# Performance work log

Measured on AMD Instinct MI355X. Metric: run time of the kernel, lower is better.

Reference implementation:

```python
import jax, jax.numpy as jnp
import numpy as np
from jax import lax

VOCAB = 50000; EMB = 128; HID = 256; NL = 9; B = 128; T = 512; H = HID // 2; PAD = 0


def setup_inputs() -> dict:
    key = jax.random.key(0)
    ks = jax.random.split(key, 16)
    p = lambda k, s: jax.random.normal(k, s, jnp.float32) * 0.05
    return {
        "chars": jax.random.randint(ks[0], (B, T), 1, VOCAB),  # in [1, VOCAB) so mask fully on
        "labels": jax.random.randint(ks[1], (B, T), 0, NL),
        "emb": p(ks[2], (VOCAB, EMB)),
        "W_ih_f": p(ks[3], (4 * H, EMB)), "W_hh_f": p(ks[4], (4 * H, H)),
        "b_ih_f": p(ks[5], (4 * H,)), "b_hh_f": p(ks[6], (4 * H,)),
        "W_ih_b": p(ks[7], (4 * H, EMB)), "W_hh_b": p(ks[8], (4 * H, H)),
        "b_ih_b": p(ks[9], (4 * H,)), "b_hh_b": p(ks[10], (4 * H,)),
        "W_out": p(ks[11], (NL, HID)), "b_out": p(ks[12], (NL,)),
        "start_trans": p(ks[13], (NL,)), "end_trans": p(ks[14], (NL,)),
        "trans": p(ks[15], (NL, NL)),
    }


def _lstm(x, Wih, Whh, bih, bhh, reverse):
    # x: (B, T, D); PyTorch gate order i, f, g, o
    bsz = x.shape[0]
    h0 = jnp.zeros((bsz, H), x.dtype)
    c0 = jnp.zeros((bsz, H), x.dtype)
    b = bih + bhh

    def step(carry, xt):
        h, c = carry
        g = xt @ Wih.T + h @ Whh.T + b  # (B, 4H)
        i, f, gg, o = jnp.split(g, 4, axis=-1)
        c = jax.nn.sigmoid(f) * c + jax.nn.sigmoid(i) * jnp.tanh(gg)
        h = jax.nn.sigmoid(o) * jnp.tanh(c)
        return (h, c), h

    _, hs = lax.scan(step, (h0, c0), jnp.swapaxes(x, 0, 1), reverse=reverse)
    return jnp.swapaxes(hs, 0, 1)  # (B, T, H)


def _crf_nll(emissions, labels, mask, start, end, trans):
    # torchcrf linear-chain CRF log-likelihood, reduction='sum'
    maskf = mask.astype(emissions.dtype)
    emit = jnp.take_along_axis(emissions, labels[..., None], 2)[..., 0]  # (B, T)
    score = start[labels[:, 0]] + (emit * maskf).sum(1)
    score = score + (trans[labels[:, :-1], labels[:, 1:]] * maskf[:, 1:]).sum(1)
    last_idx = mask.sum(1).astype(jnp.int32) - 1
    last_tags = jnp.take_along_axis(labels, last_idx[:, None], 1)[:, 0]
    score = score + end[last_tags]

    # forward algorithm (log partition) as a scan over time
    alpha0 = start[None, :] + emissions[:, 0]  # (B, L)

    def step(alpha, inp):
        e_t, m_t = inp  # (B, L), (B,)
        nxt = jax.nn.logsumexp(alpha[:, :, None] + trans[None, :, :], axis=1) + e_t
        return jnp.where(m_t[:, None], nxt, alpha), None

    alpha, _ = lax.scan(step, alpha0,
                        (jnp.swapaxes(emissions, 0, 1)[1:], jnp.swapaxes(mask, 0, 1)[1:]))
    logZ = jax.nn.logsumexp(alpha + end[None, :], axis=-1)
    return -(score - logZ).sum()


def reference(chars, labels, emb, W_ih_f, W_hh_f, b_ih_f, b_hh_f,
              W_ih_b, W_hh_b, b_ih_b, b_hh_b, W_out, b_out,
              start_trans, end_trans, trans):
    x = emb[chars]  # (B, T, EMB)
    hf = _lstm(x, W_ih_f, W_hh_f, b_ih_f, b_hh_f, False)
    hb = _lstm(x, W_ih_b, W_hh_b, b_ih_b, b_hh_b, True)
    h = jnp.concatenate([hf, hb], axis=-1)  # (B, T, HID)
    emissions = h @ W_out.T + b_out  # dropout is identity in eval mode
    mask = chars != PAD
    return _crf_nll(emissions, labels, mask, start_trans, end_trans, trans)
```

## Files before the change

kernel.cpp:

```cpp
#include <hip/hip_runtime.h>

#define B_   128
#define T_   512
#define EMB_ 128
#define H_   128
#define NL_  9
#define MT_  65536

typedef __attribute__((ext_vector_type(8))) short short8v;
typedef __attribute__((ext_vector_type(4))) float float4v;

__device__ inline unsigned short f2bf(float f){
  unsigned u = __float_as_uint(f);
  u += 0x7FFFu + ((u >> 16) & 1u);
  return (unsigned short)(u >> 16);
}
__device__ inline float bf2f(unsigned short s){
  return __uint_as_float(((unsigned)s) << 16);
}
__device__ inline float sigm(float x){ return 1.f / (1.f + __expf(-x)); }
__device__ inline float tanh_(float x){ return 2.f / (1.f + __expf(-2.f * x)) - 1.f; }

#define LOG2E 1.44269504f
__device__ inline float vexp2(float x){ float r; asm("v_exp_f32 %0, %1" : "=v"(r) : "v"(x)); return r; }
__device__ inline float vrcp (float x){ float r; asm("v_rcp_f32 %0, %1" : "=v"(r) : "v"(x)); return r; }

__device__ inline float lstm_cell(float pi, float pf, float pg, float po, float& c){
  float ei = vexp2(-LOG2E * pi);
  float ef = vexp2(-LOG2E * pf);
  float eg = vexp2( 2.f * LOG2E * pg);
  float eo = vexp2(-LOG2E * po);
  float R1 = vrcp((1.f + ei) * (1.f + eg));
  float ig = (eg - 1.f) * R1;
  float F  = vrcp(1.f + ef);
  c = fmaf(F, c, ig);
  float ec = vexp2(2.f * LOG2E * c);
  float R2 = vrcp((1.f + eo) * (1.f + ec));
  return (ec - 1.f) * R2;
}

__device__ inline void gload16(const void* g, void* l){
  __builtin_amdgcn_global_load_lds(
      (const __attribute__((address_space(1))) void*)g,
      (__attribute__((address_space(3)))       void*)l, 16, 0, 0);
}

__global__ void k0_prep(const float* __restrict__ Wihf, const float* __restrict__ Whhf,
                        const float* __restrict__ bihf, const float* __restrict__ bhhf,
                        const float* __restrict__ Wihb, const float* __restrict__ Whhb,
                        const float* __restrict__ bihb, const float* __restrict__ bhhb,
                        unsigned short* __restrict__ Wih2, unsigned short* __restrict__ Whh2,
                        float* __restrict__ biasc){
  int blk = blockIdx.x;
  int dir = blk >> 9;
  int nd  = blk & 511;
  int k   = threadIdx.x;
  int j = nd >> 2, g = nd & 3;
  int orig = g * 128 + j;
  const float* Wih = dir ? Wihb : Wihf;
  const float* Whh = dir ? Whhb : Whhf;
  Wih2[((long)(dir * 512 + nd)) * 128 + k] = f2bf(Wih[orig * EMB_ + k]);
  Whh2[((long)(dir * 512 + nd)) * 128 + k] = f2bf(Whh[orig * H_ + k]);
  if (k == 0){
    const float* bi = dir ? bihb : bihf;
    const float* bh = dir ? bhhb : bhhf;
    biasc[dir * 512 + nd] = bi[orig] + bh[orig];
  }
}

__global__ void k1_embed(const int* __restrict__ chars, const float* __restrict__ emb,
                         unsigned short* __restrict__ x){
  int i = blockIdx.x * blockDim.x + threadIdx.x;
  int m = i >> 5, q = i & 31;
  int c = chars[m];
  const float4* e4 = (const float4*)(emb + (long)c * EMB_);
  float4 v = e4[q];
  ushort4 o;
  o.x = f2bf(v.x); o.y = f2bf(v.y); o.z = f2bf(v.z); o.w = f2bf(v.w);
  *(ushort4*)(x + (long)m * EMB_ + q * 4) = o;
}

#define CST 130
__global__ __launch_bounds__(256) void k2_gemm(const unsigned short* __restrict__ x,
                                               const unsigned short* __restrict__ Wih2,
                                               const float* __restrict__ biasc,
                                               unsigned short* __restrict__ G){
  __shared__ unsigned short gsm[64 * CST];
  int w = threadIdx.x >> 6, lane = threadIdx.x & 63;
  int r = lane & 15, kb = (lane >> 4) * 8;
  long arow = (long)(blockIdx.x * 64 + w * 16 + r);
  short8v a[4];
  #pragma unroll
  for (int kf = 0; kf < 4; kf++)
    a[kf] = *(const short8v*)(x + arow * EMB_ + kf * 32 + kb);
  int ncol0 = blockIdx.y * 128;
  float4v acc[8];
  #pragma unroll
  for (int nf = 0; nf < 8; nf++){
    float4v z = {0.f, 0.f, 0.f, 0.f};
    acc[nf] = z;
    int wrow = ncol0 + nf * 16 + r;
    #pragma unroll
    for (int kf = 0; kf < 4; kf++){
      short8v bfrag = *(const short8v*)(Wih2 + (long)wrow * 128 + kf * 32 + kb);
      acc[nf] = __builtin_amdgcn_mfma_f32_16x16x32_bf16(a[kf], bfrag, acc[nf], 0, 0, 0);
    }
  }
  int rloc0 = w * 16 + (lane >> 4) * 4;
  #pragma unroll
  for (int nf = 0; nf < 8; nf++){
    int col = ncol0 + nf * 16 + r;
    float bia = biasc[col];
    #pragma unroll
    for (int reg = 0; reg < 4; reg++)
      gsm[(rloc0 + reg) * CST + nf * 16 + r] = f2bf(acc[nf][reg] + bia);
  }
  __syncthreads();
  #pragma unroll
  for (int it = 0; it < 4; it++){
    int u = it * 256 + threadIdx.x;
    int row = u >> 4, cu = u & 15;
    short8v v = *(const short8v*)&gsm[row * CST + cu * 8];
    *(short8v*)(G + (long)(blockIdx.x * 64 + row) * 1024 + ncol0 + cu * 8) = v;
  }
}

#define HBST 136
#define GSTR 520
__global__ __launch_bounds__(1024, 1) void k3_scan3(
    const unsigned short* __restrict__ G,
    const unsigned short* __restrict__ Whh2,
    unsigned short* __restrict__ hs)
{
  const int blk = blockIdx.x;
  const int dir = blk >> 3;
  const int b0  = (blk & 7) * 16;
  const int tid = threadIdx.x;
  const int w   = tid >> 6;
  const int l   = tid & 63;
  const int r   = l & 15;
  const int q   = l >> 4;

  __shared__ unsigned short hR[4][16 * HBST];
  __shared__ unsigned short Gl[2][16 * GSTR];

  short8v Wf[2][4];
  #pragma unroll
  for (int t = 0; t < 2; t++){
    const unsigned short* wp = Whh2 + ((long)(dir * 512 + 32 * w + 16 * t + r)) * 128 + q * 8;
    #pragma unroll
    for (int kf = 0; kf < 4; kf++)
      Wf[t][kf] = *(const short8v*)(wp + kf * 32);
  }

  for (int i = tid; i < 16 * HBST; i += 1024) hR[3][i] = 0;

  float cc0 = 0.f, cc1 = 0.f;
  const int j0 = 8 * w + q;
  const int j1 = j0 + 4;

  const unsigned short* Gp0 = G + ((long)(b0 + w) * T_ + (dir ? T_ - 1 : 0)) * 1024
                                + dir * 512 + l * 8;
  const long gstep = (dir ? -1L : 1L) * 1024;
  const unsigned short* Gp = Gp0 + gstep;

  gload16(Gp0, &Gl[0][w * GSTR]);
  __syncthreads();

  for (int s = 0; s < T_; s++){
    const int p = s & 1;
    if (s + 1 < T_){
      gload16(Gp, &Gl[p ^ 1][w * GSTR]);
      Gp += gstep;
    }

    const unsigned short* hrow = &hR[(s + 3) & 3][r * HBST + q * 8];
    short8v hf0 = *(const short8v*)(hrow);
    short8v hf1 = *(const short8v*)(hrow + 32);
    short8v hf2 = *(const short8v*)(hrow + 64);
    short8v hf3 = *(const short8v*)(hrow + 96);

    ushort4 gp0 = *(const ushort4*)&Gl[p][r * GSTR + 32 * w + 4 * q];
    ushort4 gp1 = *(const ushort4*)&Gl[p][r * GSTR + 32 * w + 16 + 4 * q];
    float4v acc0 = {bf2f(gp0.x), bf2f(gp0.y), bf2f(gp0.z), bf2f(gp0.w)};
    float4v acc1 = {bf2f(gp1.x), bf2f(gp1.y), bf2f(gp1.z), bf2f(gp1.w)};

    acc0 = __builtin_amdgcn_mfma_f32_16x16x32_bf16(Wf[0][0], hf0, acc0, 0, 0, 0);
    acc0 = __builtin_amdgcn_mfma_f32_16x16x32_bf16(Wf[0][1], hf1, acc0, 0, 0, 0);
    acc0 = __builtin_amdgcn_mfma_f32_16x16x32_bf16(Wf[0][2], hf2, acc0, 0, 0, 0);
    acc0 = __builtin_amdgcn_mfma_f32_16x16x32_bf16(Wf[0][3], hf3, acc0, 0, 0, 0);
    acc1 = __builtin_amdgcn_mfma_f32_16x16x32_bf16(Wf[1][0], hf0, acc1, 0, 0, 0);
    acc1 = __builtin_amdgcn_mfma_f32_16x16x32_bf16(Wf[1][1], hf1, acc1, 0, 0, 0);
    acc1 = __builtin_amdgcn_mfma_f32_16x16x32_bf16(Wf[1][2], hf2, acc1, 0, 0, 0);
    acc1 = __builtin_amdgcn_mfma_f32_16x16x32_bf16(Wf[1][3], hf3, acc1, 0, 0, 0);

    float hv0 = lstm_cell(acc0[0], acc0[1], acc0[2], acc0[3], cc0);
    float hv1 = lstm_cell(acc1[0], acc1[1], acc1[2], acc1[3], cc1);

    unsigned pk;
    asm("v_cvt_pk_bf16_f32 %0, %1, %2" : "=v"(pk) : "v"(hv0), "v"(hv1));
    unsigned short* wrow = &hR[s & 3][r * HBST];
    wrow[j0] = (unsigned short)pk;
    wrow[j1] = (unsigned short)(pk >> 16);
    __syncthreads();

    if ((s & 3) == 3){
      int ii = tid >> 8, mm = (tid >> 4) & 15, j8 = tid & 15;
      int sg = s - 3 + ii;
      int tg = dir ? (T_ - 1 - sg) : sg;
      short8v v = *(const short8v*)&hR[ii][mm * HBST + j8 * 8];
      *(short8v*)(hs + ((long)dir * MT_ + (long)(b0 + mm) * T_ + tg) * H_ + j8 * 8) = v;
      __syncthreads();
    }
  }
}

#define HSTR 264
__global__ __launch_bounds__(512) void k4_emis(const unsigned short* __restrict__ hs,
                                               const float* __restrict__ Wout,
                                               const float* __restrict__ bout,
                                               float* __restrict__ em){
  __shared__ float hcat[64 * HSTR];
  __shared__ float wo[NL_ * 256];
  int tid = threadIdx.x;
  int m0 = blockIdx.x * 64;
  const unsigned short* hf = hs;
  const unsigned short* hb = hs + (long)MT_ * H_;
  #pragma unroll
  for (int it = 0; it < 8; it++){
    int flat = it * 2048 + tid * 4;
    int r = flat >> 8, u = flat & 255;
    const unsigned short* src = (u < 128) ? (hf + (long)(m0 + r) * H_ + u)
                                          : (hb + (long)(m0 + r) * H_ + (u - 128));
    ushort4 v = *(const ushort4*)src;
    hcat[r * HSTR + u]     = bf2f(v.x);
    hcat[r * HSTR + u + 1] = bf2f(v.y);
    hcat[r * HSTR + u + 2] = bf2f(v.z);
    hcat[r * HSTR + u + 3] = bf2f(v.w);
  }
  for (int f = tid; f < NL_ * 256; f += 512) wo[f] = Wout[f];
  __syncthreads();
  #pragma unroll
  for (int half = 0; half < 2; half++){
    int idx = half * 512 + tid;
    if (idx < 64 * NL_){
      int r = idx / NL_, lbl = idx % NL_;
      float acc = bout[lbl];
      #pragma unroll 8
      for (int u = 0; u < 256; u++)
        acc = fmaf(hcat[r * HSTR + u], wo[lbl * 256 + u], acc);
      em[(long)(m0 + r) * NL_ + lbl] = acc;
    }
  }
}

__global__ void k5_crf(const float* __restrict__ em, const int* __restrict__ chars,
                       const int* __restrict__ labels, const float* __restrict__ startv,
                       const float* __restrict__ endv, const float* __restrict__ trans,
                       float* __restrict__ partial){
  int b = blockIdx.x, lane = threadIdx.x;
  const int* lab = labels + b * T_;
  const int* ch  = chars + b * T_;
  const float* e = em + (long)b * T_ * NL_;
  float sc = 0.f; int cnt = 0;
  for (int t = lane; t < T_; t += 64){
    int m = (ch[t] != 0);
    cnt += m;
    if (m){
      sc += e[t * NL_ + lab[t]];
      if (t > 0) sc += trans[lab[t - 1] * NL_ + lab[t]];
    }
  }
  #pragma unroll
  for (int off = 32; off; off >>= 1){
    sc  += __shfl_down(sc, off);
    cnt += __shfl_down(cnt, off);
  }
  sc  = __shfl(sc, 0);
  cnt = __shfl(cnt, 0);
  if (cnt < 1) cnt = 1;
  int jl = (lane < NL_) ? lane : 0;
  float tcol[NL_];
  #pragma unroll
  for (int i = 0; i < NL_; i++) tcol[i] = trans[i * NL_ + jl];
  float alpha = (lane < NL_) ? (startv[jl] + e[jl]) : -1e30f;
  float evn = (lane < NL_) ? e[NL_ + jl] : 0.f;
  int   mn  = (ch[1] != 0);
  for (int t = 1; t < T_; t++){
    float ev = evn; int m = mn;
    int t2 = (t + 1 < T_) ? t + 1 : t;
    evn = (lane < NL_) ? e[t2 * NL_ + jl] : 0.f;
    mn  = (ch[t2] != 0);
    float vv[NL_]; float mx = -1e30f;
    #pragma unroll
    for (int i = 0; i < NL_; i++){
      vv[i] = __shfl(alpha, i) + tcol[i];
      mx = fmaxf(mx, vv[i]);
    }
    float ssum = 0.f;
    #pragma unroll
    for (int i = 0; i < NL_; i++) ssum += __expf(vv[i] - mx);
    float nxt = mx + __logf(ssum) + ev;
    if (m && lane < NL_) alpha = nxt;
  }
  float av = (lane < NL_) ? (alpha + endv[jl]) : -1e30f;
  float mx = av;
  #pragma unroll
  for (int off = 8; off; off >>= 1) mx = fmaxf(mx, __shfl_down(mx, off));
  mx = __shfl(mx, 0);
  float ex = (lane < NL_) ? __expf(av - mx) : 0.f;
  #pragma unroll
  for (int off = 8; off; off >>= 1) ex += __shfl_down(ex, off);
  if (lane == 0){
    float logZ = mx + __logf(ex);
    float score = sc + startv[lab[0]] + endv[lab[cnt - 1]];
    partial[b] = logZ - score;
  }
}

__global__ void k6_reduce(const float* __restrict__ partial, float* __restrict__ out){
  int lane = threadIdx.x;
  float v = partial[lane];
  #pragma unroll
  for (int off = 32; off; off >>= 1) v += __shfl_down(v, off);
  __shared__ float tmp[2];
  if ((lane & 63) == 0) tmp[lane >> 6] = v;
  __syncthreads();
  if (lane == 0) out[0] = tmp[0] + tmp[1];
}

extern "C" void kernel_launch(void* const* d_in, const int* in_sizes, int n_in,
                              void* d_out, int out_size, void* d_ws, size_t ws_size,
                              hipStream_t stream){
  const int*   chars  = (const int*)d_in[0];
  const int*   labels = (const int*)d_in[1];
  const float* emb    = (const float*)d_in[2];
  const float* Wihf   = (const float*)d_in[3];
  const float* Whhf   = (const float*)d_in[4];
  const float* bihf   = (const float*)d_in[5];
  const float* bhhf   = (const float*)d_in[6];
  const float* Wihb   = (const float*)d_in[7];
  const float* Whhb   = (const float*)d_in[8];
  const float* bihb   = (const float*)d_in[9];
  const float* bhhb   = (const float*)d_in[10];
  const float* Wout   = (const float*)d_in[11];
  const float* bout   = (const float*)d_in[12];
  const float* startv = (const float*)d_in[13];
  const float* endv   = (const float*)d_in[14];
  const float* trans  = (const float*)d_in[15];

  char* ws = (char*)d_ws;
  unsigned short* x     = (unsigned short*)(ws);
  float*          em    = (float*)         (ws);
  float*          part  = (float*)         (ws + 2359296);
  unsigned short* Wih2  = (unsigned short*)(ws + 16777216);
  unsigned short* Whh2  = (unsigned short*)(ws + 17301504);
  float*          biasc = (float*)         (ws + 17825792);
  unsigned short* G     = (unsigned short*)(ws + 17829888);
  unsigned short* hs    = (unsigned short*)(ws + 152047616);

  hipLaunchKernelGGL(k0_prep,  dim3(1024), dim3(128), 0, stream,
                     Wihf, Whhf, bihf, bhhf, Wihb, Whhb, bihb, bhhb, Wih2, Whh2, biasc);
  hipLaunchKernelGGL(k1_embed, dim3(8192), dim3(256), 0, stream, chars, emb, x);
  hipLaunchKernelGGL(k2_gemm,  dim3(1024, 8), dim3(256), 0, stream, x, Wih2, biasc, G);
  hipLaunchKernelGGL(k3_scan3, dim3(16),   dim3(1024), 0, stream, G, Whh2, hs);
  hipLaunchKernelGGL(k4_emis,  dim3(1024), dim3(512), 0, stream, hs, Wout, bout, em);
  hipLaunchKernelGGL(k5_crf,   dim3(128),  dim3(64),  0, stream,
                     em, chars, labels, startv, endv, trans, part);
  hipLaunchKernelGGL(k6_reduce, dim3(1),   dim3(128), 0, stream, part, (float*)d_out);
}
```

Measured before the change: 957.8 us.

## Prefetch gate inputs to registers and use lightweight LDS-only barriers in LSTM scan

The recurrent scan kernel no longer stages precomputed gate inputs through LDS with async global-to-LDS loads. Each lane now loads its own gate values straight into registers, two steps ahead, in double-buffered register sets. The history buffer grows to 8 slots so the hs flush to global memory happens once per 4 steps without its own extra barrier. Per-step __syncthreads is replaced by a barrier that waits only on LDS counters, which keeps the global loads in flight across steps. The risks are more register pressure and more exposed global load latency if the prefetch distance is too short.

```diff
diff --git a/kernel.cpp b/kernel.cpp
--- a/kernel.cpp
+++ b/kernel.cpp
@@ -18,8 +18,6 @@
 __device__ inline float bf2f(unsigned short s){
   return __uint_as_float(((unsigned)s) << 16);
 }
-__device__ inline float sigm(float x){ return 1.f / (1.f + __expf(-x)); }
-__device__ inline float tanh_(float x){ return 2.f / (1.f + __expf(-2.f * x)) - 1.f; }
 
 #define LOG2E 1.44269504f
 __device__ inline float vexp2(float x){ float r; asm("v_exp_f32 %0, %1" : "=v"(r) : "v"(x)); return r; }
@@ -39,10 +37,12 @@
   return (ec - 1.f) * R2;
 }
 
-__device__ inline void gload16(const void* g, void* l){
-  __builtin_amdgcn_global_load_lds(
-      (const __attribute__((address_space(1))) void*)g,
-      (__attribute__((address_space(3)))       void*)l, 16, 0, 0);
+__device__ inline void bar(){
+  __builtin_amdgcn_sched_barrier(0);
+  asm volatile("s_waitcnt lgkmcnt(0)" ::: "memory");
+  __builtin_amdgcn_sched_barrier(0);
+  __builtin_amdgcn_s_barrier();
+  __builtin_amdgcn_sched_barrier(0);
 }
 
 __global__ void k0_prep(const float* __restrict__ Wihf, const float* __restrict__ Whhf,
@@ -126,8 +126,7 @@
 }
 
 #define HBST 136
-#define GSTR 520
-__global__ __launch_bounds__(1024, 1) void k3_scan3(
+__global__ __launch_bounds__(1024, 1) void k3_scan4(
     const unsigned short* __restrict__ G,
     const unsigned short* __restrict__ Whh2,
     unsigned short* __restrict__ hs)
@@ -141,8 +140,7 @@
   const int r   = l & 15;
   const int q   = l >> 4;
 
-  __shared__ unsigned short hR[4][16 * HBST];
-  __shared__ unsigned short Gl[2][16 * GSTR];
+  __shared__ unsigned short hR[8][16 * HBST];
 
   short8v Wf[2][4];
   #pragma unroll
@@ -152,67 +150,83 @@
     for (int kf = 0; kf < 4; kf++)
       Wf[t][kf] = *(const short8v*)(wp + kf * 32);
   }
-
-  for (int i = tid; i < 16 * HBST; i += 1024) hR[3][i] = 0;
+  #pragma unroll
+  for (int t = 0; t < 2; t++)
+    #pragma unroll
+    for (int kf = 0; kf < 4; kf++)
+      asm volatile("" : "+v"(Wf[t][kf]));
+
+  for (int i = tid; i < 16 * HBST; i += 1024) hR[7][i] = 0;
 
   float cc0 = 0.f, cc1 = 0.f;
   const int j0 = 8 * w + q;
   const int j1 = j0 + 4;
-
-  const unsigned short* Gp0 = G + ((long)(b0 + w) * T_ + (dir ? T_ - 1 : 0)) * 1024
-                                + dir * 512 + l * 8;
-  const long gstep = (dir ? -1L : 1L) * 1024;
-  const unsigned short* Gp = Gp0 + gstep;
-
-  gload16(Gp0, &Gl[0][w * GSTR]);
-  __syncthreads();
-
-  for (int s = 0; s < T_; s++){
-    const int p = s & 1;
-    if (s + 1 < T_){
-      gload16(Gp, &Gl[p ^ 1][w * GSTR]);
-      Gp += gstep;
-    }
-
-    const unsigned short* hrow = &hR[(s + 3) & 3][r * HBST + q * 8];
-    short8v hf0 = *(const short8v*)(hrow);
-    short8v hf1 = *(const short8v*)(hrow + 32);
-    short8v hf2 = *(const short8v*)(hrow + 64);
-    short8v hf3 = *(const short8v*)(hrow + 96);
-
-    ushort4 gp0 = *(const ushort4*)&Gl[p][r * GSTR + 32 * w + 4 * q];
-    ushort4 gp1 = *(const ushort4*)&Gl[p][r * GSTR + 32 * w + 16 + 4 * q];
-    float4v acc0 = {bf2f(gp0.x), bf2f(gp0.y), bf2f(gp0.z), bf2f(gp0.w)};
-    float4v acc1 = {bf2f(gp1.x), bf2f(gp1.y), bf2f(gp1.z), bf2f(gp1.w)};
-
-    acc0 = __builtin_amdgcn_mfma_f32_16x16x32_bf16(Wf[0][0], hf0, acc0, 0, 0, 0);
-    acc0 = __builtin_amdgcn_mfma_f32_16x16x32_bf16(Wf[0][1], hf1, acc0, 0, 0, 0);
-    acc0 = __builtin_amdgcn_mfma_f32_16x16x32_bf16(Wf[0][2], hf2, acc0, 0, 0, 0);
-    acc0 = __builtin_amdgcn_mfma_f32_16x16x32_bf16(Wf[0][3], hf3, acc0, 0, 0, 0);
-    acc1 = __builtin_amdgcn_mfma_f32_16x16x32_bf16(Wf[1][0], hf0, acc1, 0, 0, 0);
-    acc1 = __builtin_amdgcn_mfma_f32_16x16x32_bf16(Wf[1][1], hf1, acc1, 0, 0, 0);
-    acc1 = __builtin_amdgcn_mfma_f32_16x16x32_bf16(Wf[1][2], hf2, acc1, 0, 0, 0);
-    acc1 = __builtin_amdgcn_mfma_f32_16x16x32_bf16(Wf[1][3], hf3, acc1, 0, 0, 0);
-
-    float hv0 = lstm_cell(acc0[0], acc0[1], acc0[2], acc0[3], cc0);
-    float hv1 = lstm_cell(acc1[0], acc1[1], acc1[2], acc1[3], cc1);
-
-    unsigned pk;
-    asm("v_cvt_pk_bf16_f32 %0, %1, %2" : "=v"(pk) : "v"(hv0), "v"(hv1));
-    unsigned short* wrow = &hR[s & 3][r * HBST];
-    wrow[j0] = (unsigned short)pk;
-    wrow[j1] = (unsigned short)(pk >> 16);
-    __syncthreads();
-
-    if ((s & 3) == 3){
-      int ii = tid >> 8, mm = (tid >> 4) & 15, j8 = tid & 15;
-      int sg = s - 3 + ii;
-      int tg = dir ? (T_ - 1 - sg) : sg;
-      short8v v = *(const short8v*)&hR[ii][mm * HBST + j8 * 8];
-      *(short8v*)(hs + ((long)dir * MT_ + (long)(b0 + mm) * T_ + tg) * H_ + j8 * 8) = v;
-      __syncthreads();
-    }
-  }
+  const int fii = tid >> 8, fmm = (tid >> 4) & 15, fj8 = tid & 15;
+
+  const long gstep = dir ? -1024L : 1024L;
+  const unsigned short* gbase = G + ((long)(b0 + r) * T_ + (dir ? T_ - 1 : 0)) * 1024
+                                  + dir * 512 + 32 * w + 4 * q;
+
+#define ISSUEX(D0A, D0B, D1A, D1B, S) do{                          \
+    const unsigned short* p_ = gbase + (long)(S) * gstep;          \
+    D0A = *(const ushort4*)(p_);                                   \
+    D0B = *(const ushort4*)(p_ + 16);                              \
+    D1A = *(const ushort4*)(p_ + gstep);                           \
+    D1B = *(const ushort4*)(p_ + gstep + 16);                      \
+  }while(0)
+
+#define STEPX(S, GA, GB) do{                                       \
+    const int slot_r = ((S) + 7) & 7, slot_w = (S) & 7;            \
+    const unsigned short* hrow = &hR[slot_r][r * HBST + q * 8];    \
+    short8v hf0 = *(const short8v*)(hrow);                         \
+    short8v hf1 = *(const short8v*)(hrow + 32);                    \
+    short8v hf2 = *(const short8v*)(hrow + 64);                    \
+    short8v hf3 = *(const short8v*)(hrow + 96);                    \
+    float4v acc0 = {bf2f((GA).x), bf2f((GA).y), bf2f((GA).z), bf2f((GA).w)}; \
+    float4v acc1 = {bf2f((GB).x), bf2f((GB).y), bf2f((GB).z), bf2f((GB).w)}; \
+    acc0 = __builtin_amdgcn_mfma_f32_16x16x32_bf16(Wf[0][0], hf0, acc0, 0, 0, 0); \
+    acc0 = __builtin_amdgcn_mfma_f32_16x16x32_bf16(Wf[0][1], hf1, acc0, 0, 0, 0); \
+    acc0 = __builtin_amdgcn_mfma_f32_16x16x32_bf16(Wf[0][2], hf2, acc0, 0, 0, 0); \
+    acc0 = __builtin_amdgcn_mfma_f32_16x16x32_bf16(Wf[0][3], hf3, acc0, 0, 0, 0); \
+    acc1 = __builtin_amdgcn_mfma_f32_16x16x32_bf16(Wf[1][0], hf0, acc1, 0, 0, 0); \
+    acc1 = __builtin_amdgcn_mfma_f32_16x16x32_bf16(Wf[1][1], hf1, acc1, 0, 0, 0); \
+    acc1 = __builtin_amdgcn_mfma_f32_16x16x32_bf16(Wf[1][2], hf2, acc1, 0, 0, 0); \
+    acc1 = __builtin_amdgcn_mfma_f32_16x16x32_bf16(Wf[1][3], hf3, acc1, 0, 0, 0); \
+    float hv0 = lstm_cell(acc0[0], acc0[1], acc0[2], acc0[3], cc0);\
+    float hv1 = lstm_cell(acc1[0], acc1[1], acc1[2], acc1[3], cc1);\
+    unsigned pk_;                                                  \
+    asm("v_cvt_pk_bf16_f32 %0, %1, %2" : "=v"(pk_) : "v"(hv0), "v"(hv1)); \
+    unsigned short* wr = &hR[slot_w][r * HBST];                    \
+    wr[j0] = (unsigned short)(pk_ & 0xffffu);                      \
+    wr[j1] = (unsigned short)(pk_ >> 16);                          \
+    bar();                                                         \
+  }while(0)
+
+#define FLUSHX(S4) do{                                             \
+    int sg_ = (S4) - 4 + fii;                                      \
+    int tg_ = dir ? (T_ - 1 - sg_) : sg_;                          \
+    short8v v_ = *(const short8v*)&hR[sg_ & 7][fmm * HBST + fj8 * 8]; \
+    *(short8v*)(hs + ((long)dir * MT_ + (long)(b0 + fmm) * T_ + tg_) * H_ + fj8 * 8) = v_; \
+  }while(0)
+
+  ushort4 A0a, A0b, A1a, A1b, B0a, B0b, B1a, B1b;
+  ISSUEX(A0a, A0b, A1a, A1b, 0);
+  bar();
+
+  for (int s4 = 0; s4 < T_; s4 += 4){
+    if (s4 > 0) FLUSHX(s4);
+    ISSUEX(B0a, B0b, B1a, B1b, s4 + 2);
+    STEPX(s4 + 0, A0a, A0b);
+    STEPX(s4 + 1, A1a, A1b);
+    if (s4 + 4 < T_) ISSUEX(A0a, A0b, A1a, A1b, s4 + 4);
+    STEPX(s4 + 2, B0a, B0b);
+    STEPX(s4 + 3, B1a, B1b);
+  }
+  FLUSHX(T_);
+
+#undef ISSUEX
+#undef STEPX
+#undef FLUSHX
 }
 
 #define HSTR 264
@@ -363,7 +377,7 @@
                      Wihf, Whhf, bihf, bhhf, Wihb, Whhb, bihb, bhhb, Wih2, Whh2, biasc);
   hipLaunchKernelGGL(k1_embed, dim3(8192), dim3(256), 0, stream, chars, emb, x);
   hipLaunchKernelGGL(k2_gemm,  dim3(1024, 8), dim3(256), 0, stream, x, Wih2, biasc, G);
-  hipLaunchKernelGGL(k3_scan3, dim3(16),   dim3(1024), 0, stream, G, Whh2, hs);
+  hipLaunchKernelGGL(k3_scan4, dim3(16),   dim3(1024), 0, stream, G, Whh2, hs);
   hipLaunchKernelGGL(k4_emis,  dim3(1024), dim3(512), 0, stream, hs, Wout, bout, em);
   hipLaunchKernelGGL(k5_crf,   dim3(128),  dim3(64),  0, stream,
                      em, chars, labels, startv, endv, trans, part);
```

Result: no change. 963.0 us (+0.5%).
